# Kernel optimization log

Measured on AMD Instinct MI355X. Metric: run time of the kernel, lower is better.

## Reference

```python
import jax, jax.numpy as jnp
import numpy as np

H = 8
DQ = 32
DK = 32
DV = 32
DC = DQ + DK  # concat dim for additive attention


def setup_inputs() -> dict:
    key = jax.random.key(0)
    ks = jax.random.split(key, 8)
    bs, Lq, Lk = 2, 384, 384
    q = jax.random.normal(ks[0], (bs, Lq, H * DQ), jnp.float32)
    k = jax.random.normal(ks[1], (bs, Lk, H * DK), jnp.float32)
    v = jax.random.normal(ks[2], (bs, Lk, H * DV), jnp.float32)
    q_sequence_lengths = jax.random.randint(ks[3], (bs,), 1, Lq + 1, dtype=jnp.int32)
    k_sequence_lengths = jax.random.randint(ks[4], (bs,), 1, Lk + 1, dtype=jnp.int32)
    bound = 1.0 / np.sqrt(DC)
    w1 = jax.random.uniform(ks[5], (H, DC, DC), jnp.float32, -bound, bound)
    b1 = jax.random.uniform(ks[6], (H, DC), jnp.float32, -bound, bound)
    w2 = jax.random.uniform(ks[7], (H, DC), jnp.float32, -1.0, 1.0)
    return {"q": q, "k": k, "v": v,
            "q_sequence_lengths": q_sequence_lengths,
            "k_sequence_lengths": k_sequence_lengths,
            "w1": w1, "b1": b1, "w2": w2}


def reference(q, k, v, q_sequence_lengths, k_sequence_lengths, w1, b1, w2):
    bs, Lq, _ = q.shape
    Lk = k.shape[1]
    # split heads: (b, h, L, d)
    qh = q.reshape(bs, Lq, H, DQ).transpose(0, 2, 1, 3)
    kh = k.reshape(bs, Lk, H, DK).transpose(0, 2, 1, 3)
    vh = v.reshape(bs, Lk, H, DV).transpose(0, 2, 1, 3)
    # additive scores: tanh(cat(q_i, k_j) @ W1 + b1) @ w2
    # cat @ W1 == q @ W1[:DQ] + k @ W1[DQ:]  (avoids materializing the cat)
    qW = jnp.einsum('bhqd,hde->bhqe', qh, w1[:, :DQ, :])
    kW = jnp.einsum('bhkd,hde->bhke', kh, w1[:, DQ:, :])
    hid = jnp.tanh(qW[:, :, :, None, :] + kW[:, :, None, :, :] + b1[None, :, None, None, :])  # (b,h,q,k,DC)
    scores = jnp.einsum('bhqke,he->bhqk', hid, w2)
    # key-side length mask (end padded)
    kmask = jnp.arange(Lk)[None, :] < k_sequence_lengths[:, None]  # (b, Lk)
    scores = jnp.where(kmask[:, None, None, :], scores, jnp.float32(-1e9))
    att = jax.nn.softmax(scores, axis=-1)  # (b,h,q,k)
    out = jnp.einsum('bhqk,bhkd->bqhd', att, vh)  # (b,q,h,DV)
    # query-side length mask zeros out padded query rows
    qmask = jnp.arange(Lq)[None, :] < q_sequence_lengths[:, None]  # (b, Lq)
    out = out * qmask[:, :, None, None].astype(out.dtype)
    return out.reshape(bs, Lq, H * DV), att
```

## Files before the change

### kernel.cpp

```cpp
#include <hip/hip_runtime.h>

#define NH 8
#define LQ 384
#define LK 384
#define BS 2

__global__ __launch_bounds__(256) void pre_ek_kernel(
    const float* __restrict__ kin, const float* __restrict__ w1,
    const float* __restrict__ b1, float* __restrict__ ws)
{
    __shared__ float tile[32][65];
    const int bid = blockIdx.x;
    const int bh = bid / 12, kt = bid % 12;
    const int b = bh >> 3, h = bh & 7;
    const int k0 = kt * 32;
    const int lane = threadIdx.x & 63, w = threadIdx.x >> 6;

    float w1c[32];
    const float* w1p = w1 + (size_t)(h * 64 + 32) * 64 + lane;
    #pragma unroll
    for (int d = 0; d < 32; ++d) w1c[d] = w1p[d * 64];
    const float bv = b1[h * 64 + lane];

    #pragma unroll
    for (int s = 0; s < 8; ++s) {
        int kr = w * 8 + s;
        const float* krow = kin + ((size_t)(b * LK + k0 + kr)) * (NH * 32) + h * 32;
        float acc = bv;
        #pragma unroll
        for (int d = 0; d < 32; ++d) acc = __builtin_fmaf(krow[d], w1c[d], acc);
        tile[kr][lane] = __expf(acc + acc);
    }
    __syncthreads();
    float* wk = ws + (size_t)bh * 64 * LK + k0;
    const int k32 = lane & 31, eh = lane >> 5;
    #pragma unroll
    for (int s2 = 0; s2 < 8; ++s2) {
        int e = w * 16 + s2 * 2 + eh;
        wk[(size_t)e * LK + k32] = tile[k32][e];
    }
}

__global__ __launch_bounds__(256) void attn_kernel(
    const float* __restrict__ qin, const float* __restrict__ vin,
    const int* __restrict__ qlens, const int* __restrict__ klens,
    const float* __restrict__ w1, const float* __restrict__ w2g,
    const float* __restrict__ ws,
    float* __restrict__ outg, float* __restrict__ attg)
{
    __shared__ __align__(16) float ek[16 * LK];
    __shared__ __align__(16) float att_s[8][LK];
    __shared__ __align__(16) float eqs[8 * 64];
    __shared__ __align__(16) float w2s[64];

    const int tid = threadIdx.x, wave = tid >> 6, lane = tid & 63;
    const int bh = blockIdx.x / 48, tile = blockIdx.x % 48;
    const int b = bh >> 3, h = bh & 7;
    const int q0 = tile * 8;
    const int klen = klens[b], qlen = qlens[b];

    {
        const float4* w1g = (const float4*)(w1 + (size_t)h * 64 * 64);
        ((float4*)ek)[tid]       = w1g[tid];
        ((float4*)ek)[tid + 256] = w1g[tid + 256];
        if (tid < 64) {
            int r = tid >> 3, c = tid & 7;
            ((float4*)att_s)[tid] =
                ((const float4*)(qin + ((size_t)(b * LQ + q0 + r)) * (NH * 32) + h * 32))[c];
        } else if (tid < 80) {
            ((float4*)w2s)[tid - 64] = ((const float4*)(w2g + h * 64))[tid - 64];
        }
    }
    __syncthreads();

    {
        const float* qa = (const float*)att_s;
        float a0 = 0.f, a1 = 0.f;
        #pragma unroll
        for (int d = 0; d < 32; ++d) {
            float wv = ek[d * 64 + lane];
            a0 = __builtin_fmaf(qa[wave * 32 + d],       wv, a0);
            a1 = __builtin_fmaf(qa[(wave + 4) * 32 + d], wv, a1);
        }
        eqs[wave * 64 + lane]       = __expf(a0 + a0);
        eqs[(wave + 4) * 64 + lane] = __expf(a1 + a1);
    }

    float sc[2][6];
    #pragma unroll
    for (int i = 0; i < 2; ++i)
        #pragma unroll
        for (int j = 0; j < 6; ++j) sc[i][j] = 0.f;

    const float* ekg = ws + (size_t)bh * 64 * LK;
    const float4* eq0p = (const float4*)(eqs + (wave * 2 + 0) * 64);
    const float4* eq1p = (const float4*)(eqs + (wave * 2 + 1) * 64);

    for (int ec = 0; ec < 4; ++ec) {
        __syncthreads();
        const float4* src = (const float4*)(ekg + (size_t)ec * 16 * LK);
        #pragma unroll
        for (int r = 0; r < 6; ++r)
            ((float4*)ek)[tid + r * 256] = src[tid + r * 256];
        __syncthreads();
        #pragma unroll
        for (int q4 = 0; q4 < 4; ++q4) {
            float4 wv   = ((const float4*)w2s)[ec * 4 + q4];
            float4 eqv0 = eq0p[ec * 4 + q4];
            float4 eqv1 = eq1p[ec * 4 + q4];
            const float* ekb = ek + (q4 * 4) * LK + lane;
            #pragma unroll
            for (int j = 0; j < 6; ++j) {
                float kv0 = ekb[j * 64];
                float kv1 = ekb[LK + j * 64];
                float kv2 = ekb[2 * LK + j * 64];
                float kv3 = ekb[3 * LK + j * 64];
                {
                    float t0 = __builtin_fmaf(eqv0.x, kv0, 1.f);
                    float t1 = __builtin_fmaf(eqv0.y, kv1, 1.f);
                    float t2 = __builtin_fmaf(eqv0.z, kv2, 1.f);
                    float t3 = __builtin_fmaf(eqv0.w, kv3, 1.f);
                    float p12 = t0 * t1, p34 = t2 * t3;
                    float n12 = wv.x * t1; n12 = __builtin_fmaf(wv.y, t0, n12);
                    float n34 = wv.z * t3; n34 = __builtin_fmaf(wv.w, t2, n34);
                    float num = n12 * p34; num = __builtin_fmaf(n34, p12, num);
                    sc[0][j] = __builtin_fmaf(num, __builtin_amdgcn_rcpf(p12 * p34), sc[0][j]);
                }
                {
                    float t0 = __builtin_fmaf(eqv1.x, kv0, 1.f);
                    float t1 = __builtin_fmaf(eqv1.y, kv1, 1.f);
                    float t2 = __builtin_fmaf(eqv1.z, kv2, 1.f);
                    float t3 = __builtin_fmaf(eqv1.w, kv3, 1.f);
                    float p12 = t0 * t1, p34 = t2 * t3;
                    float n12 = wv.x * t1; n12 = __builtin_fmaf(wv.y, t0, n12);
                    float n34 = wv.z * t3; n34 = __builtin_fmaf(wv.w, t2, n34);
                    float num = n12 * p34; num = __builtin_fmaf(n34, p12, num);
                    sc[1][j] = __builtin_fmaf(num, __builtin_amdgcn_rcpf(p12 * p34), sc[1][j]);
                }
            }
        }
    }

    #pragma unroll
    for (int i = 0; i < 2; ++i) {
        int row = wave * 2 + i, q = q0 + row;
        float s_[6], p[6];
        float m = -3.4e38f;
        #pragma unroll
        for (int j = 0; j < 6; ++j) {
            int kk = j * 64 + lane;
            float v = -2.0f * sc[i][j];
            s_[j] = (kk < klen) ? v : -3.4e38f;
            m = fmaxf(m, s_[j]);
        }
        #pragma unroll
        for (int off = 32; off >= 1; off >>= 1) m = fmaxf(m, __shfl_xor(m, off));
        float ssum = 0.f;
        #pragma unroll
        for (int j = 0; j < 6; ++j) {
            int kk = j * 64 + lane;
            p[j] = (kk < klen) ? __expf(s_[j] - m) : 0.f;
            ssum += p[j];
        }
        #pragma unroll
        for (int off = 32; off >= 1; off >>= 1) ssum += __shfl_xor(ssum, off);
        float inv = __builtin_amdgcn_rcpf(ssum);
        float* arow = att_s[row];
        float* ag = attg + ((size_t)(bh * LQ + q)) * LK;
        #pragma unroll
        for (int j = 0; j < 6; ++j) {
            float a = p[j] * inv;
            arow[j * 64 + lane] = a;
            ag[j * 64 + lane]   = a;
        }
    }

    const int kf = lane >> 3, dg = lane & 7;
    float oa[2][4] = {{0.f,0.f,0.f,0.f},{0.f,0.f,0.f,0.f}};
    const float* ar0 = att_s[wave * 2 + 0];
    const float* ar1 = att_s[wave * 2 + 1];
    for (int c = 0; c < 2; ++c) {
        __syncthreads();
        const float4* vg = (const float4*)(vin + ((size_t)(b * LK + c * 192)) * (NH * 32) + h * 32);
        #pragma unroll
        for (int r = 0; r < 6; ++r) {
            int fidx = tid + r * 256;
            int kk = fidx >> 3, d4 = fidx & 7;
            ((float4*)ek)[fidx] = vg[(size_t)kk * 64 + d4];
        }
        __syncthreads();
        const float* a0p = ar0 + c * 192;
        const float* a1p = ar1 + c * 192;
        #pragma unroll 6
        for (int k0 = 0; k0 < 192; k0 += 8) {
            float4 vv = ((const float4*)ek)[(k0 + kf) * 8 + dg];
            float a0 = a0p[k0 + kf];
            float a1 = a1p[k0 + kf];
            oa[0][0] = __builtin_fmaf(a0, vv.x, oa[0][0]);
            oa[0][1] = __builtin_fmaf(a0, vv.y, oa[0][1]);
            oa[0][2] = __builtin_fmaf(a0, vv.z, oa[0][2]);
            oa[0][3] = __builtin_fmaf(a0, vv.w, oa[0][3]);
            oa[1][0] = __builtin_fmaf(a1, vv.x, oa[1][0]);
            oa[1][1] = __builtin_fmaf(a1, vv.y, oa[1][1]);
            oa[1][2] = __builtin_fmaf(a1, vv.z, oa[1][2]);
            oa[1][3] = __builtin_fmaf(a1, vv.w, oa[1][3]);
        }
    }
    #pragma unroll
    for (int i = 0; i < 2; ++i)
        #pragma unroll
        for (int u = 0; u < 4; ++u) {
            float x = oa[i][u];
            x += __shfl_xor(x, 8);
            x += __shfl_xor(x, 16);
            x += __shfl_xor(x, 32);
            oa[i][u] = x;
        }
    if (kf == 0) {
        #pragma unroll
        for (int i = 0; i < 2; ++i) {
            int q = q0 + wave * 2 + i;
            float4 o4;
            o4.x = (q < qlen) ? oa[i][0] : 0.f;
            o4.y = (q < qlen) ? oa[i][1] : 0.f;
            o4.z = (q < qlen) ? oa[i][2] : 0.f;
            o4.w = (q < qlen) ? oa[i][3] : 0.f;
            ((float4*)(outg + ((size_t)(b * LQ + q)) * (NH * 32) + h * 32))[dg] = o4;
        }
    }
}

extern "C" void kernel_launch(void* const* d_in, const int* in_sizes, int n_in,
                              void* d_out, int out_size, void* d_ws, size_t ws_size,
                              hipStream_t stream) {
    const float* q    = (const float*)d_in[0];
    const float* k    = (const float*)d_in[1];
    const float* v    = (const float*)d_in[2];
    const int*   qlen = (const int*)d_in[3];
    const int*   klen = (const int*)d_in[4];
    const float* w1   = (const float*)d_in[5];
    const float* b1   = (const float*)d_in[6];
    const float* w2   = (const float*)d_in[7];
    float* out = (float*)d_out;
    float* att = out + (size_t)BS * LQ * NH * 32;
    float* ws  = (float*)d_ws;

    pre_ek_kernel<<<192, 256, 0, stream>>>(k, w1, b1, ws);
    attn_kernel<<<768, 256, 0, stream>>>(q, v, qlen, klen, w1, w2, ws, out, att);
}
```

Baseline: 111.0 us.

## Double-buffer key-feature tiles with register prefetch and key-major layout

The precomputed exp(2·kW) workspace is now stored key-major (k, e), so the pre-kernel drops its shared-memory transpose. The attention kernel splits the keys into 64-key chunks and double-buffers them in padded shared memory, prefetching the next chunk into registers while computing. Each lane now handles one key over all 64 hidden features using float4 reads. The attention-matrix store is vectorised through shared memory, and the PV product reads V straight from global memory instead of staging it in LDS. The aim is to hide global load latency and cut barriers, at the cost of more registers and uncached global V reads.

```diff
diff --git a/kernel.cpp b/kernel.cpp
--- a/kernel.cpp
+++ b/kernel.cpp
@@ -4,12 +4,12 @@
 #define LQ 384
 #define LK 384
 #define BS 2
+#define ROWPAD 68
 
 __global__ __launch_bounds__(256) void pre_ek_kernel(
     const float* __restrict__ kin, const float* __restrict__ w1,
     const float* __restrict__ b1, float* __restrict__ ws)
 {
-    __shared__ float tile[32][65];
     const int bid = blockIdx.x;
     const int bh = bid / 12, kt = bid % 12;
     const int b = bh >> 3, h = bh & 7;
@@ -29,15 +29,7 @@
         float acc = bv;
         #pragma unroll
         for (int d = 0; d < 32; ++d) acc = __builtin_fmaf(krow[d], w1c[d], acc);
-        tile[kr][lane] = __expf(acc + acc);
-    }
-    __syncthreads();
-    float* wk = ws + (size_t)bh * 64 * LK + k0;
-    const int k32 = lane & 31, eh = lane >> 5;
-    #pragma unroll
-    for (int s2 = 0; s2 < 8; ++s2) {
-        int e = w * 16 + s2 * 2 + eh;
-        wk[(size_t)e * LK + k32] = tile[k32][e];
+        ws[((size_t)(bh * LK + k0 + kr)) * 64 + lane] = __expf(acc + acc);
     }
 }
 
@@ -48,7 +40,8 @@
     const float* __restrict__ ws,
     float* __restrict__ outg, float* __restrict__ attg)
 {
-    __shared__ __align__(16) float ek[16 * LK];
+    __shared__ __align__(16) float buf0[64 * ROWPAD];
+    __shared__ __align__(16) float buf1[64 * ROWPAD];
     __shared__ __align__(16) float att_s[8][LK];
     __shared__ __align__(16) float eqs[8 * 64];
     __shared__ __align__(16) float w2s[64];
@@ -59,10 +52,12 @@
     const int q0 = tile * 8;
     const int klen = klens[b], qlen = qlens[b];
 
+    const float* ekg = ws + (size_t)bh * LK * 64;
+
     {
         const float4* w1g = (const float4*)(w1 + (size_t)h * 64 * 64);
-        ((float4*)ek)[tid]       = w1g[tid];
-        ((float4*)ek)[tid + 256] = w1g[tid + 256];
+        ((float4*)buf1)[tid]       = w1g[tid];
+        ((float4*)buf1)[tid + 256] = w1g[tid + 256];
         if (tid < 64) {
             int r = tid >> 3, c = tid & 7;
             ((float4*)att_s)[tid] =
@@ -71,6 +66,12 @@
             ((float4*)w2s)[tid - 64] = ((const float4*)(w2g + h * 64))[tid - 64];
         }
     }
+    float4 pf[4];
+    {
+        const float4* src = (const float4*)ekg;
+        #pragma unroll
+        for (int i = 0; i < 4; ++i) pf[i] = src[tid + 256 * i];
+    }
     __syncthreads();
 
     {
@@ -78,78 +79,87 @@
         float a0 = 0.f, a1 = 0.f;
         #pragma unroll
         for (int d = 0; d < 32; ++d) {
-            float wv = ek[d * 64 + lane];
+            float wv = buf1[d * 64 + lane];
             a0 = __builtin_fmaf(qa[wave * 32 + d],       wv, a0);
             a1 = __builtin_fmaf(qa[(wave + 4) * 32 + d], wv, a1);
         }
         eqs[wave * 64 + lane]       = __expf(a0 + a0);
         eqs[(wave + 4) * 64 + lane] = __expf(a1 + a1);
     }
-
-    float sc[2][6];
-    #pragma unroll
-    for (int i = 0; i < 2; ++i)
-        #pragma unroll
-        for (int j = 0; j < 6; ++j) sc[i][j] = 0.f;
-
-    const float* ekg = ws + (size_t)bh * 64 * LK;
+    #pragma unroll
+    for (int i = 0; i < 4; ++i) {
+        int f = tid + 256 * i;
+        ((float4*)(buf0 + (f >> 4) * ROWPAD))[f & 15] = pf[i];
+    }
+    {
+        const float4* src = (const float4*)(ekg + 1 * 64 * 64);
+        #pragma unroll
+        for (int i = 0; i < 4; ++i) pf[i] = src[tid + 256 * i];
+    }
+    __syncthreads();
+
+    float sc0[6], sc1[6];
     const float4* eq0p = (const float4*)(eqs + (wave * 2 + 0) * 64);
     const float4* eq1p = (const float4*)(eqs + (wave * 2 + 1) * 64);
-
-    for (int ec = 0; ec < 4; ++ec) {
-        __syncthreads();
-        const float4* src = (const float4*)(ekg + (size_t)ec * 16 * LK);
-        #pragma unroll
-        for (int r = 0; r < 6; ++r)
-            ((float4*)ek)[tid + r * 256] = src[tid + r * 256];
-        __syncthreads();
-        #pragma unroll
-        for (int q4 = 0; q4 < 4; ++q4) {
-            float4 wv   = ((const float4*)w2s)[ec * 4 + q4];
-            float4 eqv0 = eq0p[ec * 4 + q4];
-            float4 eqv1 = eq1p[ec * 4 + q4];
-            const float* ekb = ek + (q4 * 4) * LK + lane;
+    #pragma unroll
+    for (int c = 0; c < 6; ++c) {
+        if (c < 5) {
+            float* bufn = (c & 1) ? buf0 : buf1;
             #pragma unroll
-            for (int j = 0; j < 6; ++j) {
-                float kv0 = ekb[j * 64];
-                float kv1 = ekb[LK + j * 64];
-                float kv2 = ekb[2 * LK + j * 64];
-                float kv3 = ekb[3 * LK + j * 64];
-                {
-                    float t0 = __builtin_fmaf(eqv0.x, kv0, 1.f);
-                    float t1 = __builtin_fmaf(eqv0.y, kv1, 1.f);
-                    float t2 = __builtin_fmaf(eqv0.z, kv2, 1.f);
-                    float t3 = __builtin_fmaf(eqv0.w, kv3, 1.f);
-                    float p12 = t0 * t1, p34 = t2 * t3;
-                    float n12 = wv.x * t1; n12 = __builtin_fmaf(wv.y, t0, n12);
-                    float n34 = wv.z * t3; n34 = __builtin_fmaf(wv.w, t2, n34);
-                    float num = n12 * p34; num = __builtin_fmaf(n34, p12, num);
-                    sc[0][j] = __builtin_fmaf(num, __builtin_amdgcn_rcpf(p12 * p34), sc[0][j]);
-                }
-                {
-                    float t0 = __builtin_fmaf(eqv1.x, kv0, 1.f);
-                    float t1 = __builtin_fmaf(eqv1.y, kv1, 1.f);
-                    float t2 = __builtin_fmaf(eqv1.z, kv2, 1.f);
-                    float t3 = __builtin_fmaf(eqv1.w, kv3, 1.f);
-                    float p12 = t0 * t1, p34 = t2 * t3;
-                    float n12 = wv.x * t1; n12 = __builtin_fmaf(wv.y, t0, n12);
-                    float n34 = wv.z * t3; n34 = __builtin_fmaf(wv.w, t2, n34);
-                    float num = n12 * p34; num = __builtin_fmaf(n34, p12, num);
-                    sc[1][j] = __builtin_fmaf(num, __builtin_amdgcn_rcpf(p12 * p34), sc[1][j]);
-                }
+            for (int i = 0; i < 4; ++i) {
+                int f = tid + 256 * i;
+                ((float4*)(bufn + (f >> 4) * ROWPAD))[f & 15] = pf[i];
             }
         }
+        if (c < 4) {
+            const float4* src = (const float4*)(ekg + (size_t)(c + 2) * 64 * 64);
+            #pragma unroll
+            for (int i = 0; i < 4; ++i) pf[i] = src[tid + 256 * i];
+        }
+        const float* eb = ((c & 1) ? buf1 : buf0) + lane * ROWPAD;
+        float s0 = 0.f, s1 = 0.f;
+        #pragma unroll
+        for (int e4 = 0; e4 < 16; ++e4) {
+            float4 kv = *(const float4*)(eb + 4 * e4);
+            float4 wv = ((const float4*)w2s)[e4];
+            float4 e0 = eq0p[e4];
+            float4 e1 = eq1p[e4];
+            {
+                float t0 = __builtin_fmaf(e0.x, kv.x, 1.f);
+                float t1 = __builtin_fmaf(e0.y, kv.y, 1.f);
+                float t2 = __builtin_fmaf(e0.z, kv.z, 1.f);
+                float t3 = __builtin_fmaf(e0.w, kv.w, 1.f);
+                float p12 = t0 * t1, p34 = t2 * t3;
+                float n12 = wv.x * t1; n12 = __builtin_fmaf(wv.y, t0, n12);
+                float n34 = wv.z * t3; n34 = __builtin_fmaf(wv.w, t2, n34);
+                float num = n12 * p34; num = __builtin_fmaf(n34, p12, num);
+                s0 = __builtin_fmaf(num, __builtin_amdgcn_rcpf(p12 * p34), s0);
+            }
+            {
+                float t0 = __builtin_fmaf(e1.x, kv.x, 1.f);
+                float t1 = __builtin_fmaf(e1.y, kv.y, 1.f);
+                float t2 = __builtin_fmaf(e1.z, kv.z, 1.f);
+                float t3 = __builtin_fmaf(e1.w, kv.w, 1.f);
+                float p12 = t0 * t1, p34 = t2 * t3;
+                float n12 = wv.x * t1; n12 = __builtin_fmaf(wv.y, t0, n12);
+                float n34 = wv.z * t3; n34 = __builtin_fmaf(wv.w, t2, n34);
+                float num = n12 * p34; num = __builtin_fmaf(n34, p12, num);
+                s1 = __builtin_fmaf(num, __builtin_amdgcn_rcpf(p12 * p34), s1);
+            }
+        }
+        sc0[c] = s0; sc1[c] = s1;
+        if (c < 5) __syncthreads();
     }
 
     #pragma unroll
     for (int i = 0; i < 2; ++i) {
-        int row = wave * 2 + i, q = q0 + row;
+        const float* scp = i ? sc1 : sc0;
         float s_[6], p[6];
         float m = -3.4e38f;
         #pragma unroll
         for (int j = 0; j < 6; ++j) {
             int kk = j * 64 + lane;
-            float v = -2.0f * sc[i][j];
+            float v = -2.0f * scp[j];
             s_[j] = (kk < klen) ? v : -3.4e38f;
             m = fmaxf(m, s_[j]);
         }
@@ -165,46 +175,37 @@
         #pragma unroll
         for (int off = 32; off >= 1; off >>= 1) ssum += __shfl_xor(ssum, off);
         float inv = __builtin_amdgcn_rcpf(ssum);
-        float* arow = att_s[row];
-        float* ag = attg + ((size_t)(bh * LQ + q)) * LK;
-        #pragma unroll
-        for (int j = 0; j < 6; ++j) {
-            float a = p[j] * inv;
-            arow[j * 64 + lane] = a;
-            ag[j * 64 + lane]   = a;
-        }
+        float* arow = att_s[wave * 2 + i];
+        #pragma unroll
+        for (int j = 0; j < 6; ++j) arow[j * 64 + lane] = p[j] * inv;
+    }
+
+    #pragma unroll
+    for (int i3 = 0; i3 < 3; ++i3) {
+        int f4i = i3 * 64 + lane;
+        int rl = f4i / 96, c4 = f4i % 96;
+        float4 av = *(const float4*)(&att_s[wave * 2 + rl][c4 * 4]);
+        *(float4*)(attg + ((size_t)(bh * LQ + q0 + wave * 2 + rl)) * LK + c4 * 4) = av;
     }
 
     const int kf = lane >> 3, dg = lane & 7;
+    const float* vrow = vin + (size_t)b * LK * (NH * 32) + h * 32 + kf * (NH * 32) + dg * 4;
+    const float* a0p = att_s[wave * 2 + 0];
+    const float* a1p = att_s[wave * 2 + 1];
     float oa[2][4] = {{0.f,0.f,0.f,0.f},{0.f,0.f,0.f,0.f}};
-    const float* ar0 = att_s[wave * 2 + 0];
-    const float* ar1 = att_s[wave * 2 + 1];
-    for (int c = 0; c < 2; ++c) {
-        __syncthreads();
-        const float4* vg = (const float4*)(vin + ((size_t)(b * LK + c * 192)) * (NH * 32) + h * 32);
-        #pragma unroll
-        for (int r = 0; r < 6; ++r) {
-            int fidx = tid + r * 256;
-            int kk = fidx >> 3, d4 = fidx & 7;
-            ((float4*)ek)[fidx] = vg[(size_t)kk * 64 + d4];
-        }
-        __syncthreads();
-        const float* a0p = ar0 + c * 192;
-        const float* a1p = ar1 + c * 192;
-        #pragma unroll 6
-        for (int k0 = 0; k0 < 192; k0 += 8) {
-            float4 vv = ((const float4*)ek)[(k0 + kf) * 8 + dg];
-            float a0 = a0p[k0 + kf];
-            float a1 = a1p[k0 + kf];
-            oa[0][0] = __builtin_fmaf(a0, vv.x, oa[0][0]);
-            oa[0][1] = __builtin_fmaf(a0, vv.y, oa[0][1]);
-            oa[0][2] = __builtin_fmaf(a0, vv.z, oa[0][2]);
-            oa[0][3] = __builtin_fmaf(a0, vv.w, oa[0][3]);
-            oa[1][0] = __builtin_fmaf(a1, vv.x, oa[1][0]);
-            oa[1][1] = __builtin_fmaf(a1, vv.y, oa[1][1]);
-            oa[1][2] = __builtin_fmaf(a1, vv.z, oa[1][2]);
-            oa[1][3] = __builtin_fmaf(a1, vv.w, oa[1][3]);
-        }
+    #pragma unroll 8
+    for (int k0 = 0; k0 < LK; k0 += 8) {
+        float4 vv = *(const float4*)(vrow + (size_t)k0 * (NH * 32));
+        float a0 = a0p[k0 + kf];
+        float a1 = a1p[k0 + kf];
+        oa[0][0] = __builtin_fmaf(a0, vv.x, oa[0][0]);
+        oa[0][1] = __builtin_fmaf(a0, vv.y, oa[0][1]);
+        oa[0][2] = __builtin_fmaf(a0, vv.z, oa[0][2]);
+        oa[0][3] = __builtin_fmaf(a0, vv.w, oa[0][3]);
+        oa[1][0] = __builtin_fmaf(a1, vv.x, oa[1][0]);
+        oa[1][1] = __builtin_fmaf(a1, vv.y, oa[1][1]);
+        oa[1][2] = __builtin_fmaf(a1, vv.z, oa[1][2]);
+        oa[1][3] = __builtin_fmaf(a1, vv.w, oa[1][3]);
     }
     #pragma unroll
     for (int i = 0; i < 2; ++i)
```

Measured after the change: 115.9 us. +4.4%, slower.
